# Optimization experiments

Measured on AMD Instinct MI355X. Metric: run time of the kernel, lower is better.

The kernel has to match this reference:

```python
import jax, jax.numpy as jnp
import numpy as np

C = 512
NUM_GROUPS = 32
EPS = 1e-6


def group_norm(x, gamma, beta):
    # x: [B, C, H, W]
    B, Cc, H, W = x.shape
    xg = x.reshape(B, NUM_GROUPS, Cc // NUM_GROUPS, H, W)
    mean = xg.mean(axis=(2, 3, 4), keepdims=True)
    var = xg.var(axis=(2, 3, 4), keepdims=True)
    xn = (xg - mean) / jnp.sqrt(var + EPS)
    xn = xn.reshape(B, Cc, H, W)
    return xn * gamma[None, :, None, None] + beta[None, :, None, None]


def conv1x1(x, w, b):
    # w: [out_c, in_c], x: [B, C, H, W]
    return jnp.einsum('oc,bchw->bohw', w, x) + b[None, :, None, None]


def setup_inputs() -> dict:
    key = jax.random.key(0)
    ks = jax.random.split(key, 6)
    B, H, W = 2, 64, 64
    x = jax.random.normal(ks[0], (B, C, H, W), dtype=jnp.float32)
    s = 1.0 / np.sqrt(C)
    wq = jax.random.normal(ks[1], (C, C), dtype=jnp.float32) * s
    wk = jax.random.normal(ks[2], (C, C), dtype=jnp.float32) * s
    wv = jax.random.normal(ks[3], (C, C), dtype=jnp.float32) * s
    wo = jax.random.normal(ks[4], (C, C), dtype=jnp.float32) * s
    bq = jnp.zeros((C,), jnp.float32)
    bk = jnp.zeros((C,), jnp.float32)
    bv = jnp.zeros((C,), jnp.float32)
    bo = jnp.zeros((C,), jnp.float32)
    gamma = jnp.ones((C,), jnp.float32)
    beta = jnp.zeros((C,), jnp.float32)
    return {"x": x, "gamma": gamma, "beta": beta, "wq": wq, "bq": bq,
            "wk": wk, "bk": bk, "wv": wv, "bv": bv, "wo": wo, "bo": bo}


def reference(x, gamma, beta, wq, bq, wk, bk, wv, bv, wo, bo):
    B, Cc, H, W = x.shape
    h = group_norm(x, gamma, beta)
    q = conv1x1(h, wq, bq).reshape(B, Cc, H * W)  # [B, C, N]
    k = conv1x1(h, wk, bk).reshape(B, Cc, H * W)
    v = conv1x1(h, wv, bv).reshape(B, Cc, H * W)
    scale = Cc ** (-0.5)
    # scores a[b,i,j] = sum_c q[b,c,i] * k[b,c,j]
    a = jnp.einsum('bci,bcj->bij', q, k) * scale
    a = jax.nn.softmax(a, axis=2)
    # out[b,c,i] = sum_j v[b,c,j] * a[b,i,j]  (matches bmm(v, a^T))
    o = jnp.einsum('bcj,bij->bci', v, a).reshape(B, Cc, H, W)
    o = conv1x1(o, wo, bo)
    return x + o
```

## Files before the change

kernel.cpp:

```cpp
#include <hip/hip_runtime.h>
#include <stdint.h>

#define NPIX 4096
#define CDIM 512

typedef _Float16 hv8 __attribute__((ext_vector_type(8)));
typedef float f32x4 __attribute__((ext_vector_type(4)));

__device__ __forceinline__ void lds_direct16(const _Float16* g, _Float16* l) {
    __builtin_amdgcn_global_load_lds(
        (const __attribute__((address_space(1))) void*)g,
        (__attribute__((address_space(3))) void*)l, 16, 0, 0);
}

__global__ void cvt_w(const float* __restrict__ s0, const float* __restrict__ s1,
                      const float* __restrict__ s2, const float* __restrict__ s3,
                      _Float16* __restrict__ d0, _Float16* __restrict__ d1,
                      _Float16* __restrict__ d2, _Float16* __restrict__ d3,
                      const float* __restrict__ bq, const float* __restrict__ bk,
                      float* __restrict__ bqk) {
    int i = blockIdx.x * 256 + threadIdx.x;
    d0[i] = (_Float16)s0[i];
    d1[i] = (_Float16)s1[i];
    d2[i] = (_Float16)s2[i];
    d3[i] = (_Float16)s3[i];
    if (i < 512) { bqk[i] = bq[i]; bqk[i + 512] = bk[i]; }
}

__global__ void pstats_kernel(const float* __restrict__ x,
                              float* __restrict__ partS, float* __restrict__ partQ) {
    int pb = blockIdx.x;
    int gi = pb >> 3;
    int sl = pb & 7;
    const float4* base = (const float4*)x + (long)gi * 16384 + sl * 2048;
    int tid = threadIdx.x;
    float s = 0.f, sq = 0.f;
    for (int it = 0; it < 8; ++it) {
        float4 f = base[it * 256 + tid];
        s  += f.x + f.y + f.z + f.w;
        sq += f.x * f.x + f.y * f.y + f.z * f.z + f.w * f.w;
    }
    __shared__ float rs[256], rq[256];
    rs[tid] = s; rq[tid] = sq;
    __syncthreads();
    for (int st = 128; st > 0; st >>= 1) {
        if (tid < st) { rs[tid] += rs[tid + st]; rq[tid] += rq[tid + st]; }
        __syncthreads();
    }
    if (tid == 0) { partS[pb] = rs[0]; partQ[pb] = rq[0]; }
}

__global__ void normT_kernel(const float* __restrict__ x,
                             const float* __restrict__ partS, const float* __restrict__ partQ,
                             const float* __restrict__ gamma, const float* __restrict__ beta,
                             _Float16* __restrict__ hT) {
    int b = blockIdx.z, c0 = blockIdx.x * 32, n0 = blockIdx.y * 32;
    int tid = threadIdx.x;
    __shared__ float t[32][33];
    int cl = tid >> 5;
    int nl = tid & 31;
    for (int r = 0; r < 4; ++r)
        t[r * 8 + cl][nl] = x[(long)b * CDIM * NPIX + (long)(c0 + r * 8 + cl) * NPIX + n0 + nl];
    __syncthreads();
    int c = c0 + nl;
    int gg = b * 32 + (c >> 4);
    float s = 0.f, q = 0.f;
#pragma unroll
    for (int k2 = 0; k2 < 8; ++k2) { s += partS[gg * 8 + k2]; q += partQ[gg * 8 + k2]; }
    float m    = s * (1.0f / 65536.0f);
    float rstd = rsqrtf(q * (1.0f / 65536.0f) - m * m + 1e-6f);
    float gm = gamma[c], bt = beta[c];
    for (int r = 0; r < 4; ++r) {
        int nr = r * 8 + cl;
        float val = (t[nl][nr] - m) * rstd * gm + bt;
        hT[(long)b * NPIX * CDIM + (long)(n0 + nr) * CDIM + c] = (_Float16)val;
    }
}

template<int EPI>
__launch_bounds__(256, 2)
__global__ void gemm_bt_kernel(const _Float16* __restrict__ A, const _Float16* __restrict__ BT,
                               void* __restrict__ D, const float* __restrict__ bias,
                               const float* __restrict__ resid,
                               int M, int N, int K,
                               long aBatch, long bBatch, long dBatch, long rBatch) {
    const int b = blockIdx.z;
    A  += (long)b * aBatch;
    BT += (long)b * bBatch;
    const int m0 = blockIdx.y * 128;
    const int n0 = blockIdx.x * 128;
    const int tid = threadIdx.x;
    const int l = tid & 63;
    const int w = tid >> 6;
    const int wm = (w >> 1) * 64;
    const int wn = (w & 1) * 64;
    const int lr = l & 15;
    const int lk = l >> 4;
    __shared__ __align__(16) _Float16 As[128 * 32];
    __shared__ __align__(16) _Float16 Bs[128 * 32];
    f32x4 acc[4][4] = {};
    const int nK = K >> 5;
    for (int kt = 0; kt < nK; ++kt) {
        const int kb = kt * 32;
#pragma unroll
        for (int c = 0; c < 2; ++c) {
            int chunk = c * 256 + tid;
            int row = chunk >> 2;
            int k8 = (chunk & 3) * 8;
            _Float16* ldsA = As + (size_t)(c * 256 + (tid & ~63)) * 8;
            _Float16* ldsB = Bs + (size_t)(c * 256 + (tid & ~63)) * 8;
            lds_direct16(A  + (long)(m0 + row) * K + kb + k8, ldsA);
            lds_direct16(BT + (long)(n0 + row) * K + kb + k8, ldsB);
        }
        __syncthreads();
        hv8 af[4], bfr[4];
#pragma unroll
        for (int mi = 0; mi < 4; ++mi)
            af[mi] = *(const hv8*)(As + (size_t)(wm + mi * 16 + lr) * 32 + lk * 8);
#pragma unroll
        for (int ni = 0; ni < 4; ++ni)
            bfr[ni] = *(const hv8*)(Bs + (size_t)(wn + ni * 16 + lr) * 32 + lk * 8);
#pragma unroll
        for (int mi = 0; mi < 4; ++mi)
#pragma unroll
            for (int ni = 0; ni < 4; ++ni)
                acc[mi][ni] = __builtin_amdgcn_mfma_f32_16x16x32_f16(af[mi], bfr[ni], acc[mi][ni], 0, 0, 0);
        __syncthreads();
    }
#pragma unroll
    for (int mi = 0; mi < 4; ++mi)
#pragma unroll
        for (int ni = 0; ni < 4; ++ni)
#pragma unroll
            for (int r = 0; r < 4; ++r) {
                int row = m0 + wm + mi * 16 + lk * 4 + r;
                int col = n0 + wn + ni * 16 + lr;
                float val = acc[mi][ni][r];
                if (EPI == 0) {
                    ((_Float16*)D)[(long)b * dBatch + (long)row * N + col] = (_Float16)(val + bias[col]);
                } else if (EPI == 1) {
                    ((_Float16*)D)[(long)b * dBatch + (long)row * N + col] = (_Float16)(val + bias[row]);
                } else if (EPI == 2) {
                    long idx = (long)row * N + col;
                    ((float*)D)[(long)b * dBatch + idx] =
                        val + bias[row] + resid[(long)b * rBatch + idx];
                } else {
                    long qoff = (long)(col >> 9) * (2L * NPIX * CDIM);
                    ((_Float16*)D)[qoff + (long)b * dBatch + (long)row * CDIM + (col & 511)] =
                        (_Float16)(val + bias[col]);
                }
            }
}

__launch_bounds__(512, 2)
__global__ void attn_kernel(const _Float16* __restrict__ qT, const _Float16* __restrict__ kT,
                            const _Float16* __restrict__ v,
                            _Float16* __restrict__ p0, _Float16* __restrict__ p1,
                            float* __restrict__ lbuf) {
    __shared__ __align__(16) _Float16 Ks[2][32 * 512];
    __shared__ __align__(16) char ps[2][64 * 80];
    __shared__ float red[8][64];
    __shared__ float redt[64];

    const int g = blockIdx.x;
    const int xcd = g & 7;
    const int comb = xcd >> 1;
    const int itile = ((g >> 3) << 1) | (xcd & 1);
    const int batch = comb >> 1;
    const int jhalf = comb & 1;
    const int i0 = itile * 64;
    const int jbase = jhalf * 2048;

    const int tid = threadIdx.x;
    const int l = tid & 63, w = tid >> 6;
    const int lr = l & 15, lk = l >> 4;
    const int iq = w >> 1, jq = w & 1;

    const _Float16* qb = qT + (long)batch * NPIX * CDIM;
    const _Float16* kb = kT + (long)batch * NPIX * CDIM;
    const _Float16* vb = v  + (long)batch * CDIM * NPIX;

    hv8 af[16];
    {
        const _Float16* qr = qb + (long)(i0 + iq * 16 + lr) * CDIM + lk * 8;
#pragma unroll
        for (int kk = 0; kk < 16; ++kk)
            af[kk] = *(const hv8*)(qr + kk * 32);
    }

    f32x4 oacc[4][4] = {};
    float lsum[4] = {};
    hv8 vf[4];

    const _Float16* vptr = vb + (long)(w * 64 + lr) * NPIX + jbase + lk * 8;
    const float scale = 0.044194173824159216f;

#define STAGE(BUF, JT)                                                               \
    {                                                                                \
        const long j0s = (long)jbase + (JT) * 32;                                    \
        _Float16* kd = Ks[BUF];                                                      \
        _Pragma("unroll")                                                            \
        for (int q = 0; q < 4; ++q) {                                                \
            int row = q * 8 + w;                                                     \
            int cc = l ^ (row & 7);                                                  \
            lds_direct16(kb + (j0s + row) * CDIM + cc * 8, kd + row * 512);          \
        }                                                                            \
    }

#define VLOAD(JT)                                                                    \
    {                                                                                \
        _Pragma("unroll")                                                            \
        for (int ni = 0; ni < 4; ++ni)                                               \
            vf[ni] = *(const hv8*)(vptr + (long)ni * (16 * NPIX) + (JT) * 32);       \
    }

#define QKEXP(CUR)                                                                   \
    {                                                                                \
        const char* kbase = (const char*)Ks[CUR];                                    \
        f32x4 sa = {}, sb = {};                                                      \
        const int jj = jq * 16 + lr;                                                 \
        const uint32_t sw = (uint32_t)((jj & 7) << 4);                               \
        _Pragma("unroll")                                                            \
        for (int kk = 0; kk < 8; ++kk) {                                             \
            hv8 b0 = *(const hv8*)(kbase + (((uint32_t)(jj * 1024 + (2 * kk) * 64 + lk * 16)) ^ sw));     \
            sa = __builtin_amdgcn_mfma_f32_16x16x32_f16(af[2 * kk], b0, sa, 0, 0, 0);                     \
            hv8 b1 = *(const hv8*)(kbase + (((uint32_t)(jj * 1024 + (2 * kk + 1) * 64 + lk * 16)) ^ sw)); \
            sb = __builtin_amdgcn_mfma_f32_16x16x32_f16(af[2 * kk + 1], b1, sb, 0, 0, 0);                 \
        }                                                                            \
        sa += sb;                                                                    \
        _Pragma("unroll")                                                            \
        for (int r = 0; r < 4; ++r) {                                                \
            float p = __expf(sa[r] * scale);                                         \
            lsum[r] += p;                                                            \
            int i = iq * 16 + lk * 4 + r;                                            \
            int j2 = jq * 16 + lr;                                                   \
            *(_Float16*)(ps[CUR] + i * 80 + j2 * 2) = (_Float16)p;                   \
        }                                                                            \
    }

#define PVSTEP(PRV)                                                                  \
    {                                                                                \
        _Pragma("unroll")                                                            \
        for (int mi = 0; mi < 4; ++mi) {                                             \
            int i2 = mi * 16 + lr;                                                   \
            hv8 pa = *(const hv8*)(ps[PRV] + i2 * 80 + lk * 16);                     \
            _Pragma("unroll")                                                        \
            for (int ni = 0; ni < 4; ++ni)                                           \
                oacc[mi][ni] = __builtin_amdgcn_mfma_f32_16x16x32_f16(pa, vf[ni], oacc[mi][ni], 0, 0, 0); \
        }                                                                            \
    }

#define ENDBAR(N)                                                                    \
    __builtin_amdgcn_sched_barrier(0);                                               \
    asm volatile("s_waitcnt vmcnt(" #N ") lgkmcnt(0)" ::: "memory");                 \
    __builtin_amdgcn_s_barrier();                                                    \
    __builtin_amdgcn_sched_barrier(0);

#define STEP(JT, CUR)                                                                \
    {                                                                                \
        if ((JT) < 63) STAGE((CUR) ^ 1, (JT) + 1)                                    \
        __builtin_amdgcn_sched_barrier(0);                                           \
        __builtin_amdgcn_s_setprio(1);                                               \
        QKEXP(CUR)                                                                   \
        PVSTEP((CUR) ^ 1)                                                            \
        __builtin_amdgcn_s_setprio(0);                                               \
        __builtin_amdgcn_sched_barrier(0);                                           \
        VLOAD(JT)                                                                    \
        ENDBAR(4)                                                                    \
    }

    STAGE(0, 0)
    __builtin_amdgcn_sched_barrier(0);
    asm volatile("s_waitcnt vmcnt(0)" ::: "memory");
    __builtin_amdgcn_s_barrier();
    __builtin_amdgcn_sched_barrier(0);

    STAGE(1, 1)
    __builtin_amdgcn_s_setprio(1);
    QKEXP(0)
    __builtin_amdgcn_s_setprio(0);
    VLOAD(0)
    ENDBAR(4)

    for (int jt = 1; jt < 63; jt += 2) {
        STEP(jt,     1)
        STEP(jt + 1, 0)
    }
    STEP(63, 1)

    asm volatile("s_waitcnt vmcnt(0)" ::: "memory");
    __builtin_amdgcn_sched_barrier(0);
    PVSTEP(1)

#pragma unroll
    for (int m = 1; m <= 8; m <<= 1)
#pragma unroll
        for (int r = 0; r < 4; ++r)
            lsum[r] += __shfl_xor(lsum[r], m, 64);
    if (lr == 0)
#pragma unroll
        for (int r = 0; r < 4; ++r)
            red[w][iq * 16 + lk * 4 + r] = lsum[r];
    __syncthreads();
    if (tid < 64) {
        int iq2 = tid >> 4;
        float lv = red[iq2 * 2][tid] + red[iq2 * 2 + 1][tid];
        redt[tid] = 1.0f / lv;
        lbuf[jhalf * 8192 + batch * NPIX + i0 + tid] = lv;
    }
    __syncthreads();

    _Float16* dsth = (jhalf ? p1 : p0) + (long)batch * NPIX * CDIM;
#pragma unroll
    for (int mi = 0; mi < 4; ++mi)
#pragma unroll
        for (int r = 0; r < 4; ++r) {
            int row = mi * 16 + lk * 4 + r;
            float rv = redt[row];
#pragma unroll
            for (int ni = 0; ni < 4; ++ni) {
                int c = w * 64 + ni * 16 + lr;
                dsth[(long)(i0 + row) * CDIM + c] = (_Float16)(oacc[mi][ni][r] * rv);
            }
        }
#undef STEP
#undef ENDBAR
#undef PVSTEP
#undef QKEXP
#undef VLOAD
#undef STAGE
}

__global__ void combine_kernel(const _Float16* __restrict__ p0, const _Float16* __restrict__ p1,
                               const float* __restrict__ lbuf, _Float16* __restrict__ out) {
    long g = (long)blockIdx.x * 256 + threadIdx.x;
    long base = g * 8;
    int rowg = (int)(g >> 6);
    float l0 = lbuf[rowg], l1 = lbuf[8192 + rowg];
    float w0 = l0 / (l0 + l1);
    float w1 = 1.0f - w0;
    hv8 a = *(const hv8*)(p0 + base);
    hv8 b = *(const hv8*)(p1 + base);
    hv8 o;
#pragma unroll
    for (int i = 0; i < 8; ++i)
        o[i] = (_Float16)((float)a[i] * w0 + (float)b[i] * w1);
    *(hv8*)(out + base) = o;
}

extern "C" void kernel_launch(void* const* d_in, const int* in_sizes, int n_in,
                              void* d_out, int out_size, void* d_ws, size_t ws_size,
                              hipStream_t stream) {
    const float* x     = (const float*)d_in[0];
    const float* gamma = (const float*)d_in[1];
    const float* beta  = (const float*)d_in[2];
    const float* wq    = (const float*)d_in[3];
    const float* bq    = (const float*)d_in[4];
    const float* wk    = (const float*)d_in[5];
    const float* bk    = (const float*)d_in[6];
    const float* wv    = (const float*)d_in[7];
    const float* bv    = (const float*)d_in[8];
    const float* wo    = (const float*)d_in[9];
    const float* bo    = (const float*)d_in[10];
    float* out = (float*)d_out;

    char* ws = (char*)d_ws;
    float* partS = (float*)ws;
    float* partQ = partS + 512;
    float* bqk   = partQ + 512;
    _Float16* wqb = (_Float16*)(ws + 8192);
    _Float16* wkb = wqb + 262144;
    _Float16* wvb = wkb + 262144;
    _Float16* wob = wvb + 262144;
    _Float16* hT  = wob + 262144;
    const long TSZ = (long)2 * NPIX * CDIM;
    _Float16* qT = hT + TSZ;
    _Float16* kT = qT + TSZ;
    _Float16* vv = kT + TSZ;
    _Float16* oT = vv + TSZ;
    float* lbuf = (float*)(oT + TSZ);

    cvt_w<<<dim3(1024), dim3(256), 0, stream>>>(wq, wk, wv, wo, wqb, wkb, wvb, wob,
                                                bq, bk, bqk);
    pstats_kernel<<<dim3(512), dim3(256), 0, stream>>>(x, partS, partQ);
    normT_kernel<<<dim3(16, 128, 2), dim3(256), 0, stream>>>(x, partS, partQ, gamma, beta, hT);

    const long NC = (long)NPIX * CDIM;
    gemm_bt_kernel<3><<<dim3(8, 32, 2), dim3(256), 0, stream>>>(
        hT, wqb, (void*)qT, bqk, nullptr, NPIX, 1024, CDIM, NC, 0L, NC, 0L);
    gemm_bt_kernel<1><<<dim3(32, 4, 2), dim3(256), 0, stream>>>(
        wvb, hT, (void*)vv, bv, nullptr, CDIM, NPIX, CDIM, 0L, NC, NC, 0L);

    attn_kernel<<<dim3(256), dim3(512), 0, stream>>>(qT, kT, vv, oT, hT, lbuf);

    combine_kernel<<<dim3(2048), dim3(256), 0, stream>>>(oT, hT, lbuf, qT);

    gemm_bt_kernel<2><<<dim3(32, 4, 2), dim3(256), 0, stream>>>(
        wob, qT, (void*)out, bo, x, CDIM, NPIX, CDIM, 0L, NC, NC, NC);
}
```

Measured before the change: 181.5 us.

## Fuse split-KV combine into output projection GEMM and weight cast into stats

Removes the separate combine kernel by merging the two partial attention outputs, weighted by their softmax sums, while staging the B operand of the final output-projection GEMM. It also folds the fp16 weight conversion and bias packing into the group-norm statistics kernel, removing two launches and one full fp16 intermediate write and read. In exchange, the final GEMM reads two partial tensors through registers instead of one tensor via direct-to-LDS loads. Each partial is re-read by every M-tile block (4 times), and the B tile is now staged through registers.

```diff
diff --git a/kernel.cpp b/kernel.cpp
--- a/kernel.cpp
+++ b/kernel.cpp
@@ -13,27 +13,31 @@
         (__attribute__((address_space(3))) void*)l, 16, 0, 0);
 }
 
-__global__ void cvt_w(const float* __restrict__ s0, const float* __restrict__ s1,
-                      const float* __restrict__ s2, const float* __restrict__ s3,
-                      _Float16* __restrict__ d0, _Float16* __restrict__ d1,
-                      _Float16* __restrict__ d2, _Float16* __restrict__ d3,
-                      const float* __restrict__ bq, const float* __restrict__ bk,
-                      float* __restrict__ bqk) {
-    int i = blockIdx.x * 256 + threadIdx.x;
-    d0[i] = (_Float16)s0[i];
-    d1[i] = (_Float16)s1[i];
-    d2[i] = (_Float16)s2[i];
-    d3[i] = (_Float16)s3[i];
-    if (i < 512) { bqk[i] = bq[i]; bqk[i + 512] = bk[i]; }
-}
-
 __global__ void pstats_kernel(const float* __restrict__ x,
-                              float* __restrict__ partS, float* __restrict__ partQ) {
+                              float* __restrict__ partS, float* __restrict__ partQ,
+                              const float* __restrict__ wq, const float* __restrict__ wk,
+                              const float* __restrict__ wv, const float* __restrict__ wo,
+                              _Float16* __restrict__ d0, _Float16* __restrict__ d1,
+                              _Float16* __restrict__ d2, _Float16* __restrict__ d3,
+                              const float* __restrict__ bq, const float* __restrict__ bk,
+                              float* __restrict__ bqk) {
     int pb = blockIdx.x;
+    int tid = threadIdx.x;
+
+#pragma unroll
+    for (int h = 0; h < 2; ++h) {
+        int ii = pb * 512 + h * 256 + tid;
+        d0[ii] = (_Float16)wq[ii];
+        d1[ii] = (_Float16)wk[ii];
+        d2[ii] = (_Float16)wv[ii];
+        d3[ii] = (_Float16)wo[ii];
+        if (ii < 512) bqk[ii] = bq[ii];
+        else if (ii < 1024) bqk[ii] = bk[ii - 512];
+    }
+
     int gi = pb >> 3;
     int sl = pb & 7;
     const float4* base = (const float4*)x + (long)gi * 16384 + sl * 2048;
-    int tid = threadIdx.x;
     float s = 0.f, sq = 0.f;
     for (int it = 0; it < 8; ++it) {
         float4 f = base[it * 256 + tid];
@@ -81,9 +85,8 @@
 __launch_bounds__(256, 2)
 __global__ void gemm_bt_kernel(const _Float16* __restrict__ A, const _Float16* __restrict__ BT,
                                void* __restrict__ D, const float* __restrict__ bias,
-                               const float* __restrict__ resid,
                                int M, int N, int K,
-                               long aBatch, long bBatch, long dBatch, long rBatch) {
+                               long aBatch, long bBatch, long dBatch) {
     const int b = blockIdx.z;
     A  += (long)b * aBatch;
     BT += (long)b * bBatch;
@@ -136,19 +139,95 @@
                 int row = m0 + wm + mi * 16 + lk * 4 + r;
                 int col = n0 + wn + ni * 16 + lr;
                 float val = acc[mi][ni][r];
-                if (EPI == 0) {
-                    ((_Float16*)D)[(long)b * dBatch + (long)row * N + col] = (_Float16)(val + bias[col]);
-                } else if (EPI == 1) {
+                if (EPI == 1) {
                     ((_Float16*)D)[(long)b * dBatch + (long)row * N + col] = (_Float16)(val + bias[row]);
-                } else if (EPI == 2) {
-                    long idx = (long)row * N + col;
-                    ((float*)D)[(long)b * dBatch + idx] =
-                        val + bias[row] + resid[(long)b * rBatch + idx];
                 } else {
                     long qoff = (long)(col >> 9) * (2L * NPIX * CDIM);
                     ((_Float16*)D)[qoff + (long)b * dBatch + (long)row * CDIM + (col & 511)] =
                         (_Float16)(val + bias[col]);
                 }
+            }
+}
+
+__launch_bounds__(256, 2)
+__global__ void gemm_final_kernel(const _Float16* __restrict__ A,
+                                  const _Float16* __restrict__ p0,
+                                  const _Float16* __restrict__ p1,
+                                  const float* __restrict__ lbuf,
+                                  float* __restrict__ D, const float* __restrict__ bias,
+                                  const float* __restrict__ resid) {
+    const int b = blockIdx.z;
+    const int m0 = blockIdx.y * 128;
+    const int n0 = blockIdx.x * 128;
+    const int tid = threadIdx.x;
+    const int l = tid & 63;
+    const int w = tid >> 6;
+    const int wm = (w >> 1) * 64;
+    const int wn = (w & 1) * 64;
+    const int lr = l & 15;
+    const int lk = l >> 4;
+    __shared__ __align__(16) _Float16 As[128 * 32];
+    __shared__ __align__(16) _Float16 Bs[128 * 32];
+    __shared__ float wA[128], wB[128];
+
+    if (tid < 128) {
+        int rowg = b * NPIX + n0 + tid;
+        float l0 = lbuf[rowg], l1 = lbuf[8192 + rowg];
+        float inv = 1.0f / (l0 + l1);
+        wA[tid] = l0 * inv;
+        wB[tid] = l1 * inv;
+    }
+    __syncthreads();
+
+    const _Float16* pb0 = p0 + (long)b * NPIX * CDIM;
+    const _Float16* pb1 = p1 + (long)b * NPIX * CDIM;
+
+    f32x4 acc[4][4] = {};
+    for (int kt = 0; kt < 16; ++kt) {
+        const int kb = kt * 32;
+#pragma unroll
+        for (int c = 0; c < 2; ++c) {
+            int chunk = c * 256 + tid;
+            int row = chunk >> 2;
+            int k8 = (chunk & 3) * 8;
+            _Float16* ldsA = As + (size_t)(c * 256 + (tid & ~63)) * 8;
+            lds_direct16(A + (long)(m0 + row) * CDIM + kb + k8, ldsA);
+            long goff = (long)(n0 + row) * CDIM + kb + k8;
+            hv8 va = *(const hv8*)(pb0 + goff);
+            hv8 vb = *(const hv8*)(pb1 + goff);
+            float w0 = wA[row], w1 = wB[row];
+            hv8 vo;
+#pragma unroll
+            for (int i = 0; i < 8; ++i)
+                vo[i] = (_Float16)((float)va[i] * w0 + (float)vb[i] * w1);
+            *(hv8*)(Bs + (size_t)chunk * 8) = vo;
+        }
+        __syncthreads();
+        hv8 af[4], bfr[4];
+#pragma unroll
+        for (int mi = 0; mi < 4; ++mi)
+            af[mi] = *(const hv8*)(As + (size_t)(wm + mi * 16 + lr) * 32 + lk * 8);
+#pragma unroll
+        for (int ni = 0; ni < 4; ++ni)
+            bfr[ni] = *(const hv8*)(Bs + (size_t)(wn + ni * 16 + lr) * 32 + lk * 8);
+#pragma unroll
+        for (int mi = 0; mi < 4; ++mi)
+#pragma unroll
+            for (int ni = 0; ni < 4; ++ni)
+                acc[mi][ni] = __builtin_amdgcn_mfma_f32_16x16x32_f16(af[mi], bfr[ni], acc[mi][ni], 0, 0, 0);
+        __syncthreads();
+    }
+#pragma unroll
+    for (int mi = 0; mi < 4; ++mi)
+#pragma unroll
+        for (int ni = 0; ni < 4; ++ni)
+#pragma unroll
+            for (int r = 0; r < 4; ++r) {
+                int row = m0 + wm + mi * 16 + lk * 4 + r;
+                int col = n0 + wn + ni * 16 + lr;
+                long idx = (long)row * NPIX + col;
+                D[(long)b * NPIX * CDIM + idx] =
+                    acc[mi][ni][r] + bias[row] + resid[(long)b * NPIX * CDIM + idx];
             }
 }
 
@@ -331,23 +410,6 @@
 #undef STAGE
 }
 
-__global__ void combine_kernel(const _Float16* __restrict__ p0, const _Float16* __restrict__ p1,
-                               const float* __restrict__ lbuf, _Float16* __restrict__ out) {
-    long g = (long)blockIdx.x * 256 + threadIdx.x;
-    long base = g * 8;
-    int rowg = (int)(g >> 6);
-    float l0 = lbuf[rowg], l1 = lbuf[8192 + rowg];
-    float w0 = l0 / (l0 + l1);
-    float w1 = 1.0f - w0;
-    hv8 a = *(const hv8*)(p0 + base);
-    hv8 b = *(const hv8*)(p1 + base);
-    hv8 o;
-#pragma unroll
-    for (int i = 0; i < 8; ++i)
-        o[i] = (_Float16)((float)a[i] * w0 + (float)b[i] * w1);
-    *(hv8*)(out + base) = o;
-}
-
 extern "C" void kernel_launch(void* const* d_in, const int* in_sizes, int n_in,
                               void* d_out, int out_size, void* d_ws, size_t ws_size,
                               hipStream_t stream) {
@@ -380,21 +442,18 @@
     _Float16* oT = vv + TSZ;
     float* lbuf = (float*)(oT + TSZ);
 
-    cvt_w<<<dim3(1024), dim3(256), 0, stream>>>(wq, wk, wv, wo, wqb, wkb, wvb, wob,
-                                                bq, bk, bqk);
-    pstats_kernel<<<dim3(512), dim3(256), 0, stream>>>(x, partS, partQ);
+    pstats_kernel<<<dim3(512), dim3(256), 0, stream>>>(
+        x, partS, partQ, wq, wk, wv, wo, wqb, wkb, wvb, wob, bq, bk, bqk);
     normT_kernel<<<dim3(16, 128, 2), dim3(256), 0, stream>>>(x, partS, partQ, gamma, beta, hT);
 
     const long NC = (long)NPIX * CDIM;
     gemm_bt_kernel<3><<<dim3(8, 32, 2), dim3(256), 0, stream>>>(
-        hT, wqb, (void*)qT, bqk, nullptr, NPIX, 1024, CDIM, NC, 0L, NC, 0L);
+        hT, wqb, (void*)qT, bqk, NPIX, 1024, CDIM, NC, 0L, NC);
     gemm_bt_kernel<1><<<dim3(32, 4, 2), dim3(256), 0, stream>>>(
-        wvb, hT, (void*)vv, bv, nullptr, CDIM, NPIX, CDIM, 0L, NC, NC, 0L);
+        wvb, hT, (void*)vv, bv, CDIM, NPIX, CDIM, 0L, NC, NC);
 
     attn_kernel<<<dim3(256), dim3(512), 0, stream>>>(qT, kT, vv, oT, hT, lbuf);
 
-    combine_kernel<<<dim3(2048), dim3(256), 0, stream>>>(oT, hT, lbuf, qT);
-
-    gemm_bt_kernel<2><<<dim3(32, 4, 2), dim3(256), 0, stream>>>(
-        wob, qT, (void*)out, bo, x, CDIM, NPIX, CDIM, 0L, NC, NC, NC);
-}
+    gemm_final_kernel<<<dim3(32, 4, 2), dim3(256), 0, stream>>>(
+        wob, oT, hT, lbuf, out, bo, x);
+}
```

Measured after the change: 177.8 us. -2.1%, faster.
